# Performance work log

Hardware: AMD Instinct MI355X
Metric: run time of the kernel (lower is better)

The kernel has to match this reference:

```python
import jax, jax.numpy as jnp
import numpy as np

B, T, D, HS = 8, 2048, 768, 64
H = D // HS  # 12 heads
LN_EPS = 1e-5


def setup_inputs() -> dict:
    key = jax.random.key(0)
    ks = jax.random.split(key, 8)
    s = 0.02
    x = jax.random.normal(ks[0], (B, T, D), jnp.float32)
    Wx = jax.random.normal(ks[1], (D, D), jnp.float32) * s
    Ww = jax.random.normal(ks[2], (D, D), jnp.float32) * 0.01  # w_proj.weight ~ N(0,0.01)
    # w_proj bias schedule: logit(1 - linspace(0.9,0.999,H)) per head, expanded over head_size
    r_sched = jnp.linspace(0.9, 0.999, H)
    w_target = 1.0 - r_sched
    bw = jnp.log(w_target / (1.0 - w_target))          # logit
    bw = jnp.repeat(bw[:, None], HS, axis=1).reshape(-1)  # (D,)
    Wk = jax.random.normal(ks[3], (D, D), jnp.float32) * s
    Wv = jax.random.normal(ks[4], (D, D), jnp.float32) * s
    Wr = jax.random.normal(ks[5], (D, D), jnp.float32) * s
    Wo = jax.random.normal(ks[6], (D, D), jnp.float32) * s
    gamma = jnp.ones((D,), jnp.float32)
    beta = jnp.zeros((D,), jnp.float32)
    return {"x": x, "Wx": Wx, "Ww": Ww, "bw": bw, "Wk": Wk, "Wv": Wv,
            "Wr": Wr, "Wo": Wo, "gamma": gamma, "beta": beta}


def _layernorm(x, gamma, beta):
    mu = jnp.mean(x, axis=-1, keepdims=True)
    var = jnp.mean(jnp.square(x - mu), axis=-1, keepdims=True)
    return (x - mu) * jax.lax.rsqrt(var + LN_EPS) * gamma + beta


def _selective_scan(k, v, w):
    """k,v,w: (T,B,H,HS). State S: (B,H,HS,HS).
    S_t = (1 - w_t) * S_{t-1} (decay along key dim) + k_t (x) v_t;  y_t = k_t . S_t."""
    S0 = jnp.zeros((B, H, HS, HS), k.dtype)

    def step(S, inp):
        kt, vt, wt = inp  # each (B,H,HS)
        S = S * (1.0 - wt)[..., :, None] + kt[..., :, None] * vt[..., None, :]
        yt = jnp.einsum('bhi,bhij->bhj', kt, S)
        return S, yt

    _, ys = jax.lax.scan(step, S0, (k, v, w))
    return ys  # (T,B,H,HS)


def reference(x, Wx, Ww, bw, Wk, Wv, Wr, Wo, gamma, beta):
    xn = _layernorm(x, gamma, beta)                       # (B,T,D)
    xp = jnp.einsum('btd,ed->bte', xn, Wx)                # x_proj
    w = jax.nn.sigmoid(jnp.einsum('bte,fe->btf', xp, Ww) + bw)
    k = jnp.einsum('btd,ed->bte', xn, Wk)
    v = jnp.einsum('btd,ed->bte', xn, Wv)
    r = jax.nn.sigmoid(jnp.einsum('btd,ed->bte', xn, Wr))

    def to_scan(a):  # (B,T,D) -> (T,B,H,HS)
        return a.reshape(B, T, H, HS).transpose(1, 0, 2, 3)

    ys = _selective_scan(to_scan(k), to_scan(v), to_scan(w))  # (T,B,H,HS)
    y = ys.transpose(1, 0, 2, 3).reshape(B, T, D)
    y = y * r
    return jnp.einsum('btd,ed->bte', y, Wo)
```

## Files before the change

kernel.cpp:

```cpp
#include <hip/hip_runtime.h>

#define B_ 8
#define T_ 2048
#define D_ 768
#define H_ 12
#define HS_ 64
#define LN_EPS 1e-5f
#define NC 32
#define TC 64

typedef __attribute__((ext_vector_type(8))) short bf16x8;
typedef __attribute__((ext_vector_type(4))) float f32x4;

__device__ __forceinline__ ushort f2bf(float f) {
  unsigned u = __builtin_bit_cast(unsigned, f);
  unsigned r = (u + 0x7FFFu + ((u >> 16) & 1u)) >> 16;
  return (ushort)r;
}
__device__ __forceinline__ float bf2f(ushort u) {
  return __builtin_bit_cast(float, ((unsigned)u) << 16);
}

__device__ __forceinline__ int fragaddr(int t, int i) {
  return ((t >> 4) * 2 + (i >> 5)) * 512 + ((((i >> 3) & 3) * 16) + (t & 15)) * 8 + (i & 7);
}
__device__ __forceinline__ int fragswz(int i) {
  return (((i >> 3) & 3) << 3) ^ (((i >> 5) & 1) << 5);
}

__global__ __launch_bounds__(256) void zero_out_kernel(float* __restrict__ out, int n) {
  for (int i = blockIdx.x * 256 + threadIdx.x; i < n; i += gridDim.x * 256)
    out[i] = 0.f;
}

__global__ __launch_bounds__(256) void prep_kernel(
    const float* __restrict__ w0, const float* __restrict__ w1,
    const float* __restrict__ w2, const float* __restrict__ w3,
    const float* __restrict__ w4, const float* __restrict__ Wx,
    ushort* __restrict__ dst, ushort* __restrict__ WxT) {
  if (blockIdx.y < 5) {
    const float* srcs[5] = {w0, w1, w2, w3, w4};
    const int slots[5] = {0, 1, 2, 4, 5};
    const float* src = srcs[blockIdx.y];
    ushort* d = dst + (size_t)slots[blockIdx.y] * 589824;
    int idx = (blockIdx.x * 256 + threadIdx.x) * 4;
    float4 v = *reinterpret_cast<const float4*>(src + idx);
    ushort4 o;
    o.x = f2bf(v.x); o.y = f2bf(v.y); o.z = f2bf(v.z); o.w = f2bf(v.w);
    *reinterpret_cast<ushort4*>(d + idx) = o;
  } else {
    __shared__ ushort tile[32][33];
    const int bx = (blockIdx.x % 24) * 32;
    const int by = (blockIdx.x / 24) * 32;
    const int tx = threadIdx.x & 31, ty = threadIdx.x >> 5;
#pragma unroll
    for (int r = 0; r < 32; r += 8)
      tile[ty + r][tx] = f2bf(Wx[(size_t)(by + ty + r) * 768 + bx + tx]);
    __syncthreads();
#pragma unroll
    for (int r = 0; r < 32; r += 8)
      WxT[(size_t)(bx + ty + r) * 768 + by + tx] = tile[tx][ty + r];
  }
}

__global__ __launch_bounds__(256) void ln_kernel(
    const float* __restrict__ x, const float* __restrict__ gamma,
    const float* __restrict__ beta, ushort* __restrict__ xn) {
  const int wv = threadIdx.x >> 6;
  const int lane = threadIdx.x & 63;
  const int row = blockIdx.x * 4 + wv;
  const float* xr = x + (size_t)row * D_;
  float4 a[3];
#pragma unroll
  for (int s = 0; s < 3; ++s)
    a[s] = *reinterpret_cast<const float4*>(xr + s * 256 + lane * 4);
  float sum = 0.f;
#pragma unroll
  for (int s = 0; s < 3; ++s) sum += a[s].x + a[s].y + a[s].z + a[s].w;
#pragma unroll
  for (int off = 32; off; off >>= 1) sum += __shfl_xor(sum, off);
  float mu = sum * (1.f / 768.f);
  float vs = 0.f;
#pragma unroll
  for (int s = 0; s < 3; ++s) {
    float dx = a[s].x - mu, dy = a[s].y - mu, dz = a[s].z - mu, dw = a[s].w - mu;
    vs += dx * dx + dy * dy + dz * dz + dw * dw;
  }
#pragma unroll
  for (int off = 32; off; off >>= 1) vs += __shfl_xor(vs, off);
  float rs = rsqrtf(vs * (1.f / 768.f) + LN_EPS);
  ushort* orow = xn + (size_t)row * D_;
#pragma unroll
  for (int s = 0; s < 3; ++s) {
    int col = s * 256 + lane * 4;
    float4 g = *reinterpret_cast<const float4*>(gamma + col);
    float4 bb = *reinterpret_cast<const float4*>(beta + col);
    ushort4 o;
    o.x = f2bf((a[s].x - mu) * rs * g.x + bb.x);
    o.y = f2bf((a[s].y - mu) * rs * g.y + bb.y);
    o.z = f2bf((a[s].z - mu) * rs * g.z + bb.z);
    o.w = f2bf((a[s].w - mu) * rs * g.w + bb.w);
    *reinterpret_cast<ushort4*>(orow + col) = o;
  }
}

__global__ __launch_bounds__(512, 2) void gemm256(
    const ushort* __restrict__ A, const ushort* __restrict__ W,
    float* __restrict__ Cf,
    ushort* __restrict__ d0, ushort* __restrict__ d1,
    ushort* __restrict__ d2, ushort* __restrict__ d3, int mode) {
  __shared__ __align__(16) ushort lds[65536];
  const int tid = threadIdx.x;
  const int wid = tid >> 6;
  const int lane = tid & 63;
  const int wr = wid >> 2, wc = wid & 3;
  const int fr = lane & 15, fq = lane >> 4;
  const int m0 = blockIdx.x * 256, n0 = blockIdx.y * 256;
  const int strow = tid >> 3;
  const int stblk = tid & 7;

  const int RA0 = wr * 8192;
  const int RA1 = 32768 + wr * 8192;
  const int RB0 = 16384 + (wc >> 1) * 8192 + (wc & 1) * 4096;
  const int RB1 = 49152 + (wc >> 1) * 8192 + (wc & 1) * 4096;

  f32x4 acc[8][4];
#pragma unroll
  for (int m = 0; m < 8; ++m)
#pragma unroll
    for (int n = 0; n < 4; ++n) acc[m][n] = (f32x4){0.f, 0.f, 0.f, 0.f};

#define STAGE_HALF(gb, grow0, kk0, roff)                                          \
  {                                                                               \
    _Pragma("unroll") for (int j = 0; j < 2; ++j) {                               \
      const int lr_ = j * 64 + strow;                                             \
      const int bs_ = stblk ^ (lr_ & 7);                                          \
      const ushort* s_ = (gb) + (size_t)((grow0) + lr_) * 768 + (kk0) + bs_ * 8;  \
      __builtin_amdgcn_global_load_lds(                                           \
          (const __attribute__((address_space(1))) void*)s_,                      \
          (__attribute__((address_space(3))) void*)(lds + (roff) + j * 4096 + wid * 512), \
          16, 0, 0);                                                              \
    }                                                                             \
  }

#define LDF(dst, base, rf, kk)                                                    \
  dst = *reinterpret_cast<const bf16x8*>(                                         \
      lds + (base) + ((rf)*16 + fr) * 64 + ((((kk)*4 + fq) ^ (fr & 7)) * 8));

#define MFMA_Q(mb, nb, aa, bb)                                                    \
  _Pragma("unroll") for (int m_ = 0; m_ < 4; ++m_)                                \
  _Pragma("unroll") for (int n_ = 0; n_ < 2; ++n_)                                \
  _Pragma("unroll") for (int k_ = 0; k_ < 2; ++k_)                                \
    acc[(mb) + m_][(nb) + n_] = __builtin_amdgcn_mfma_f32_16x16x32_bf16(          \
        aa[m_][k_], bb[n_][k_], acc[(mb) + m_][(nb) + n_], 0, 0, 0);

#define LDF_AL(RA) \
  _Pragma("unroll") for (int m = 0; m < 4; ++m) { LDF(aL[m][0], RA, m, 0); LDF(aL[m][1], RA, m, 1); }
#define LDF_AH(RA) \
  _Pragma("unroll") for (int m = 0; m < 4; ++m) { LDF(aH[m][0], RA, m + 4, 0); LDF(aH[m][1], RA, m + 4, 1); }
#define LDF_BL(RB) \
  _Pragma("unroll") for (int n = 0; n < 2; ++n) { LDF(bL[n][0], RB, n, 0); LDF(bL[n][1], RB, n, 1); }
#define LDF_BH(RB) \
  _Pragma("unroll") for (int n = 0; n < 2; ++n) { LDF(bH[n][0], RB, n + 2, 0); LDF(bH[n][1], RB, n + 2, 1); }

  STAGE_HALF(A, m0, 0, 0);
  STAGE_HALF(A, m0 + 128, 0, 8192);
  STAGE_HALF(W, n0, 0, 16384);
  STAGE_HALF(W, n0 + 128, 0, 24576);
  STAGE_HALF(W, n0, 64, 49152);
  STAGE_HALF(W, n0 + 128, 64, 57344);
  asm volatile("s_waitcnt vmcnt(4)" ::: "memory");
  __builtin_amdgcn_s_barrier();

  bf16x8 aL[4][2], aH[4][2], bL[2][2], bH[2][2];

  for (int i = 0; i < 6; ++i) {
    const int kQ = (2 * i + 1) * 64;
    const int kP2 = (2 * i + 2 <= 11 ? 2 * i + 2 : 11) * 64;
    const int kQ2 = (2 * i + 3 <= 11 ? 2 * i + 3 : 11) * 64;

    STAGE_HALF(A, m0, kQ, 32768);
    STAGE_HALF(A, m0 + 128, kQ, 40960);
    LDF_AL(RA0);
    LDF_BL(RB0);
    LDF_BH(RB0);
    __builtin_amdgcn_s_barrier();
    __builtin_amdgcn_s_setprio(1);
    MFMA_Q(0, 0, aL, bL);
    MFMA_Q(0, 2, aL, bH);
    __builtin_amdgcn_s_setprio(0);
    __builtin_amdgcn_s_barrier();
    STAGE_HALF(W, n0, kP2, 16384);
    STAGE_HALF(W, n0 + 128, kP2, 24576);
    LDF_AH(RA0);
    __builtin_amdgcn_s_barrier();
    __builtin_amdgcn_s_setprio(1);
    MFMA_Q(4, 0, aH, bL);
    MFMA_Q(4, 2, aH, bH);
    __builtin_amdgcn_s_setprio(0);
    asm volatile("s_waitcnt vmcnt(4)" ::: "memory");
    __builtin_amdgcn_s_barrier();

    STAGE_HALF(A, m0, kP2, 0);
    STAGE_HALF(A, m0 + 128, kP2, 8192);
    LDF_AL(RA1);
    LDF_BL(RB1);
    LDF_BH(RB1);
    __builtin_amdgcn_s_barrier();
    __builtin_amdgcn_s_setprio(1);
    MFMA_Q(0, 0, aL, bL);
    MFMA_Q(0, 2, aL, bH);
    __builtin_amdgcn_s_setprio(0);
    __builtin_amdgcn_s_barrier();
    STAGE_HALF(W, n0, kQ2, 49152);
    STAGE_HALF(W, n0 + 128, kQ2, 57344);
    LDF_AH(RA1);
    __builtin_amdgcn_s_barrier();
    __builtin_amdgcn_s_setprio(1);
    MFMA_Q(4, 0, aH, bL);
    MFMA_Q(4, 2, aH, bH);
    __builtin_amdgcn_s_setprio(0);
    asm volatile("s_waitcnt vmcnt(4)" ::: "memory");
    __builtin_amdgcn_s_barrier();
  }

  const int r0 = fq * 4;
  if (mode == 5) {
    const int sel = n0 >= 2304 ? 3 : n0 >= 1536 ? 2 : n0 >= 768 ? 1 : 0;
    const int nb = n0 - sel * 768;
    if (sel == 1) {
#pragma unroll
      for (int mf = 0; mf < 8; ++mf)
#pragma unroll
        for (int nf = 0; nf < 4; ++nf) {
          int gr = m0 + wr * 128 + mf * 16 + r0;
          int gc = nb + wc * 64 + nf * 16 + fr;
          int b = gr >> 11, t = gr & 2047;
          int c = t >> 6, s0 = t & 63;
          int h = gc >> 6, j = gc & 63;
          size_t addr = ((size_t)((b * 12 + h) * 32 + c)) * 4096 +
                        (size_t)(((j >> 4) * 2 + (s0 >> 5)) * 512 +
                                 (((s0 >> 3) & 3) * 16 + (j & 15)) * 8 + (s0 & 7));
          ushort4 o;
          o.x = f2bf(acc[mf][nf][0]); o.y = f2bf(acc[mf][nf][1]);
          o.z = f2bf(acc[mf][nf][2]); o.w = f2bf(acc[mf][nf][3]);
          *reinterpret_cast<ushort4*>(d1 + addr) = o;
        }
    } else if (sel == 2) {
#pragma unroll
      for (int mf = 0; mf < 8; ++mf)
#pragma unroll
        for (int nf = 0; nf < 4; ++nf) {
          int gr = m0 + wr * 128 + mf * 16 + r0;
          int gc = nb + wc * 64 + nf * 16 + fr;
          int b = gr >> 11, t = gr & 2047;
          int c = t >> 6, tin = t & 63;
          int h = gc >> 6, j = gc & 63;
          size_t addr = ((size_t)((b * 12 + h) * 32 + c)) * 4096 +
                        (size_t)(((tin >> 4) * 64 + ((tin >> 2) & 3) * 16 + (j & 15)) * 16 +
                                 (j >> 4) * 4);
          ushort4 o;
          o.x = f2bf(1.f / (1.f + __expf(-acc[mf][nf][0])));
          o.y = f2bf(1.f / (1.f + __expf(-acc[mf][nf][1])));
          o.z = f2bf(1.f / (1.f + __expf(-acc[mf][nf][2])));
          o.w = f2bf(1.f / (1.f + __expf(-acc[mf][nf][3])));
          *reinterpret_cast<ushort4*>(d2 + addr) = o;
        }
    } else {
      ushort* dst = sel == 0 ? d0 : d3;
#pragma unroll
      for (int mf = 0; mf < 8; ++mf)
#pragma unroll
        for (int nf = 0; nf < 4; ++nf) {
          int gr = m0 + wr * 128 + mf * 16 + r0;
          int gc = nb + wc * 64 + nf * 16 + fr;
#pragma unroll
          for (int rr = 0; rr < 4; ++rr)
            dst[(size_t)(gr + rr) * 768 + gc] = f2bf(acc[mf][nf][rr]);
        }
    }
  } else {
#pragma unroll
    for (int mf = 0; mf < 8; ++mf)
#pragma unroll
      for (int nf = 0; nf < 4; ++nf) {
        int gr = m0 + wr * 128 + mf * 16 + r0;
        int gc = n0 + wc * 64 + nf * 16 + fr;
#pragma unroll
        for (int rr = 0; rr < 4; ++rr)
          Cf[(size_t)(gr + rr) * 768 + gc] = acc[mf][nf][rr];
      }
  }
#undef STAGE_HALF
#undef LDF
#undef MFMA_Q
#undef LDF_AL
#undef LDF_AH
#undef LDF_BL
#undef LDF_BH
}

__global__ __launch_bounds__(256) void scan_mc3(
    const ushort* __restrict__ kb, const ushort* __restrict__ zb,
    const ushort* __restrict__ vbF, const float* __restrict__ bwp,
    ushort* __restrict__ McT, float* __restrict__ aend) {
  __shared__ ushort kt[64 * 72];
  __shared__ ushort zt[64 * 72];
  __shared__ ushort kIAfA[4096];
  __shared__ float part[256];
  const int bh = blockIdx.x, c = blockIdx.y;
  const int b = bh / H_, h = bh % H_;
  const int tid = threadIdx.x;
  const int w = tid >> 6, lane = tid & 63;
  const int fr = lane & 15, fq = lane >> 4;
  const int row = tid >> 2, c16 = (tid & 3) * 16;
  const float bwh = bwp[h * 64];

  {
    const ushort* gk = kb + ((size_t)(b * T_ + c * TC + row)) * 768 + h * 64 + c16;
    const ushort* gz = zb + ((size_t)(b * T_ + c * TC + row)) * 768 + h * 64 + c16;
    uint4 k0 = *(const uint4*)gk, k1 = *(const uint4*)(gk + 8);
    uint4 z0 = *(const uint4*)gz, z1 = *(const uint4*)(gz + 8);
    *reinterpret_cast<uint4*>(&kt[row * 72 + c16]) = k0;
    *reinterpret_cast<uint4*>(&kt[row * 72 + c16 + 8]) = k1;
    *reinterpret_cast<uint4*>(&zt[row * 72 + c16]) = z0;
    *reinterpret_cast<uint4*>(&zt[row * 72 + c16 + 8]) = z1;
  }
  bf16x8 vfr[8];
  {
    const ushort* vch = vbF + ((size_t)bh * NC + c) * 4096;
#pragma unroll
    for (int f = 0; f < 8; ++f)
      vfr[f] = *reinterpret_cast<const bf16x8*>(vch + f * 512 + lane * 8);
  }
  __syncthreads();
  float dreg[16];
  float p = 1.f;
#pragma unroll
  for (int tt = 0; tt < 16; ++tt) {
    float z = bf2f(zt[(w * 16 + tt) * 72 + lane]);
    float d = 1.f / (1.f + __expf(z + bwh));
    dreg[tt] = d;
    p *= d;
  }
  part[w * 64 + lane] = p;
  __syncthreads();
  float a = 1.f;
  for (int w2 = 0; w2 < w; ++w2) a *= part[w2 * 64 + lane];
  if (w == 0)
    aend[((size_t)bh * NC + c) * 64 + lane] =
        part[lane] * part[64 + lane] * part[128 + lane] * part[192 + lane];
#pragma unroll
  for (int tt = 0; tt < 16; ++tt) {
    int t = w * 16 + tt;
    float k = bf2f(kt[t * 72 + lane]);
    a *= dreg[tt];
    kIAfA[fragaddr(lane, t)] = f2bf(k / a);
  }
  __syncthreads();

  bf16x8 af2[2];
#pragma unroll
  for (int kk = 0; kk < 2; ++kk)
    af2[kk] = *reinterpret_cast<const bf16x8*>(&kIAfA[(w * 2 + kk) * 512 + lane * 8]);
  f32x4 accM[4];
#pragma unroll
  for (int nf = 0; nf < 4; ++nf) accM[nf] = (f32x4){0.f, 0.f, 0.f, 0.f};
#pragma unroll
  for (int kk = 0; kk < 2; ++kk)
#pragma unroll
    for (int nf = 0; nf < 4; ++nf)
      accM[nf] = __builtin_amdgcn_mfma_f32_16x16x32_bf16(af2[kk], vfr[nf * 2 + kk], accM[nf], 0, 0, 0);
  ushort* mch = McT + ((size_t)bh * NC + c) * 4096;
#pragma unroll
  for (int nf = 0; nf < 4; ++nf) {
    ushort4 o;
    o.x = f2bf(accM[nf][0]); o.y = f2bf(accM[nf][1]);
    o.z = f2bf(accM[nf][2]); o.w = f2bf(accM[nf][3]);
    *reinterpret_cast<ushort4*>(&mch[(nf * 16 + fr) * 64 + w * 16 + fq * 4]) = o;
  }
}

__global__ __launch_bounds__(256) void scan_chain3(
    const ushort* __restrict__ McT, const float* __restrict__ aend,
    ushort* __restrict__ S0F) {
  const int bh = blockIdx.x;
  const int j = threadIdx.x >> 2;
  const int i0 = blockIdx.y * 32 + (threadIdx.x & 3) * 8;
  const int fbase = ((j >> 4) * 2 + (i0 >> 5)) * 512 + (((i0 >> 3) & 3) * 16 + (j & 15)) * 8;
  const ushort* mbase = McT + ((size_t)bh * NC) * 4096 + j * 64 + i0;
  const float* abase = aend + ((size_t)bh * NC) * 64 + i0;
  float S[8];
#pragma unroll
  for (int p = 0; p < 8; ++p) S[p] = 0.f;

  ushort4 m0 = *reinterpret_cast<const ushort4*>(mbase);
  ushort4 m1 = *reinterpret_cast<const ushort4*>(mbase + 4);
  float4 a0 = *(const float4*)(abase);
  float4 a1 = *(const float4*)(abase + 4);

  for (int c = 0; c < NC; ++c) {
    int cn = c + 1 < NC ? c + 1 : NC - 1;
    ushort4 n0 = *reinterpret_cast<const ushort4*>(mbase + (size_t)cn * 4096);
    ushort4 n1 = *reinterpret_cast<const ushort4*>(mbase + (size_t)cn * 4096 + 4);
    float4 b0 = *(const float4*)(abase + (size_t)cn * 64);
    float4 b1 = *(const float4*)(abase + (size_t)cn * 64 + 4);

    ushort* s0 = S0F + ((size_t)bh * NC + c) * 4096 + fbase;
    ushort4 o0, o1;
    o0.x = f2bf(S[0]); o0.y = f2bf(S[1]); o0.z = f2bf(S[2]); o0.w = f2bf(S[3]);
    o1.x = f2bf(S[4]); o1.y = f2bf(S[5]); o1.z = f2bf(S[6]); o1.w = f2bf(S[7]);
    *reinterpret_cast<ushort4*>(s0) = o0;
    *reinterpret_cast<ushort4*>(s0 + 4) = o1;

    S[0] = a0.x * (S[0] + bf2f(m0.x));
    S[1] = a0.y * (S[1] + bf2f(m0.y));
    S[2] = a0.z * (S[2] + bf2f(m0.z));
    S[3] = a0.w * (S[3] + bf2f(m0.w));
    S[4] = a1.x * (S[4] + bf2f(m1.x));
    S[5] = a1.y * (S[5] + bf2f(m1.y));
    S[6] = a1.z * (S[6] + bf2f(m1.z));
    S[7] = a1.w * (S[7] + bf2f(m1.w));

    m0 = n0; m1 = n1; a0 = b0; a1 = b1;
  }
}

__global__ __launch_bounds__(256, 2) void scan_y3(
    const ushort* __restrict__ kb, const ushort* __restrict__ zb,
    const ushort* __restrict__ vbF, const ushort* __restrict__ rbF,
    const ushort* __restrict__ S0F, const float* __restrict__ bwp,
    ushort* __restrict__ yrow) {
  __shared__ ushort kt[64 * 72];
  __shared__ ushort zt[64 * 72];
  __shared__ ushort kAf[4096];
  __shared__ ushort kIAfB[4096];
  __shared__ ushort Am[64 * 72];
  __shared__ float part[256];
  const int bh = blockIdx.x, c = blockIdx.y;
  const int b = bh / H_, h = bh % H_;
  const int tid = threadIdx.x;
  const int w = tid >> 6, lane = tid & 63;
  const int fr = lane & 15, fq = lane >> 4;
  const int row = tid >> 2, c16 = (tid & 3) * 16;
  const float bwh = bwp[h * 64];
  const int swz = fragswz(lane);

  {
    const ushort* gk = kb + ((size_t)(b * T_ + c * TC + row)) * 768 + h * 64 + c16;
    const ushort* gz = zb + ((size_t)(b * T_ + c * TC + row)) * 768 + h * 64 + c16;
    uint4 k0 = *(const uint4*)gk, k1 = *(const uint4*)(gk + 8);
    uint4 z0 = *(const uint4*)gz, z1 = *(const uint4*)(gz + 8);
    *reinterpret_cast<uint4*>(&kt[row * 72 + c16]) = k0;
    *reinterpret_cast<uint4*>(&kt[row * 72 + c16 + 8]) = k1;
    *reinterpret_cast<uint4*>(&zt[row * 72 + c16]) = z0;
    *reinterpret_cast<uint4*>(&zt[row * 72 + c16 + 8]) = z1;
  }
  bf16x8 vfr[8], s0fr[8];
  {
    const ushort* vch = vbF + ((size_t)bh * NC + c) * 4096;
    const ushort* s0ch = S0F + ((size_t)bh * NC + c) * 4096;
#pragma unroll
    for (int f = 0; f < 8; ++f) {
      vfr[f] = *reinterpret_cast<const bf16x8*>(vch + f * 512 + lane * 8);
      s0fr[f] = *reinterpret_cast<const bf16x8*>(s0ch + f * 512 + lane * 8);
    }
  }
  ushort4 rp0, rp1, rp2, rp3;
  {
    const ushort* rch = rbF + ((size_t)bh * NC + c) * 4096 + tid * 16;
    rp0 = *reinterpret_cast<const ushort4*>(rch);
    rp1 = *reinterpret_cast<const ushort4*>(rch + 4);
    rp2 = *reinterpret_cast<const ushort4*>(rch + 8);
    rp3 = *reinterpret_cast<const ushort4*>(rch + 12);
  }
  const ushort rl[16] = {rp0.x, rp0.y, rp0.z, rp0.w, rp1.x, rp1.y, rp1.z, rp1.w,
                         rp2.x, rp2.y, rp2.z, rp2.w, rp3.x, rp3.y, rp3.z, rp3.w};
  __syncthreads();
  float dreg[16];
  float p = 1.f;
#pragma unroll
  for (int tt = 0; tt < 16; ++tt) {
    float z = bf2f(zt[(w * 16 + tt) * 72 + lane]);
    float d = 1.f / (1.f + __expf(z + bwh));
    dreg[tt] = d;
    p *= d;
  }
  part[w * 64 + lane] = p;
  __syncthreads();
  float a = 1.f;
  for (int w2 = 0; w2 < w; ++w2) a *= part[w2 * 64 + lane];
#pragma unroll
  for (int tt = 0; tt < 16; ++tt) {
    int t = w * 16 + tt;
    float k = bf2f(kt[t * 72 + lane]);
    a *= dreg[tt];
    int ad = fragaddr(t, lane) ^ swz;
    kAf[ad] = f2bf(k * a);
    kIAfB[ad] = f2bf(k / a);
  }
  __syncthreads();

  bf16x8 af[2];
#pragma unroll
  for (int kk = 0; kk < 2; ++kk) {
    int ra = ((w * 2 + kk) * 512 + lane * 8) ^ (((lane >> 4) << 3) ^ (kk << 5));
    af[kk] = *reinterpret_cast<const bf16x8*>(&kAf[ra]);
  }
  {
    f32x4 accA[4];
#pragma unroll
    for (int nf = 0; nf < 4; ++nf) accA[nf] = (f32x4){0.f, 0.f, 0.f, 0.f};
#pragma unroll
    for (int kk = 0; kk < 2; ++kk)
#pragma unroll
      for (int nf = 0; nf < 4; ++nf) {
        int rb8 = ((nf * 2 + kk) * 512 + lane * 8) ^ (((lane >> 4) << 3) ^ (kk << 5));
        bf16x8 b8 = *reinterpret_cast<const bf16x8*>(&kIAfB[rb8]);
        accA[nf] = __builtin_amdgcn_mfma_f32_16x16x32_bf16(af[kk], b8, accA[nf], 0, 0, 0);
      }
#pragma unroll
    for (int nf = 0; nf < 4; ++nf)
#pragma unroll
      for (int q = 0; q < 4; ++q) {
        int t = w * 16 + fq * 4 + q;
        int s = nf * 16 + fr;
        Am[t * 72 + s] = f2bf((s <= t) ? accA[nf][q] : 0.f);
      }
  }
  __syncthreads();

  f32x4 accY[4];
#pragma unroll
  for (int nf = 0; nf < 4; ++nf) accY[nf] = (f32x4){0.f, 0.f, 0.f, 0.f};
#pragma unroll
  for (int kk = 0; kk < 2; ++kk)
#pragma unroll
    for (int nf = 0; nf < 4; ++nf)
      accY[nf] = __builtin_amdgcn_mfma_f32_16x16x32_bf16(af[kk], s0fr[nf * 2 + kk], accY[nf], 0, 0, 0);
#pragma unroll
  for (int kk = 0; kk < 2; ++kk) {
    bf16x8 am8 = *reinterpret_cast<const bf16x8*>(&Am[(w * 16 + fr) * 72 + kk * 32 + fq * 8]);
#pragma unroll
    for (int nf = 0; nf < 4; ++nf)
      accY[nf] = __builtin_amdgcn_mfma_f32_16x16x32_bf16(am8, vfr[nf * 2 + kk], accY[nf], 0, 0, 0);
  }
#pragma unroll
  for (int nf = 0; nf < 4; ++nf)
#pragma unroll
    for (int q = 0; q < 4; ++q) {
      int t = w * 16 + fq * 4 + q;
      int j = nf * 16 + fr;
      size_t go = ((size_t)(b * T_ + c * TC + t)) * 768 + h * 64 + j;
      yrow[go] = f2bf(accY[nf][q] * bf2f(rl[nf * 4 + q]));
    }
}

extern "C" void kernel_launch(void* const* d_in, const int* in_sizes, int n_in,
                              void* d_out, int out_size, void* d_ws, size_t ws_size,
                              hipStream_t stream) {
  const float* x     = (const float*)d_in[0];
  const float* Wx    = (const float*)d_in[1];
  const float* Ww    = (const float*)d_in[2];
  const float* bw    = (const float*)d_in[3];
  const float* Wk    = (const float*)d_in[4];
  const float* Wv    = (const float*)d_in[5];
  const float* Wr    = (const float*)d_in[6];
  const float* Wo    = (const float*)d_in[7];
  const float* gamma = (const float*)d_in[8];
  const float* beta  = (const float*)d_in[9];
  float* out = (float*)d_out;

  const size_t NEED = 208404480ull;
  if (ws_size < NEED) {
    zero_out_kernel<<<2048, 256, 0, stream>>>(out, out_size);
    return;
  }

  char* ws = (char*)d_ws;
  ushort* xn  = (ushort*)ws;
  ushort* wb  = (ushort*)(ws + 25165824);
  ushort* WxT = (ushort*)(ws + 32243712);
  ushort* kb  = (ushort*)(ws + 57409536);
  ushort* vbF = (ushort*)(ws + 82575360);
  ushort* rbF = (ushort*)(ws + 107741184);
  ushort* yr  = (ushort*)(ws + 132907008);
  ushort* zb  = (ushort*)(ws + 158072832);
  ushort* McT = (ushort*)ws;
  ushort* S0F = (ushort*)(ws + 32243712);
  float*  aendb = (float*)(ws + 132907008);

  ushort* WcatB = wb;
  ushort* Mb  = wb + 3 * 589824;
  ushort* WoB = wb + 4 * 589824;
  ushort* WwB = wb + 5 * 589824;

  prep_kernel<<<dim3(576, 6), 256, 0, stream>>>(Wk, Wv, Wr, Wo, Ww, Wx, wb, WxT);
  gemm256<<<dim3(3, 3), 512, 0, stream>>>(WwB, WxT, nullptr, Mb, nullptr, nullptr,
                                          nullptr, 5);
  ln_kernel<<<4096, 256, 0, stream>>>(x, gamma, beta, xn);

  gemm256<<<dim3(64, 12), 512, 0, stream>>>(xn, WcatB, nullptr, kb, vbF, rbF, zb, 5);

  scan_mc3<<<dim3(96, NC), 256, 0, stream>>>(kb, zb, vbF, bw, McT, aendb);
  scan_chain3<<<dim3(96, 2), 256, 0, stream>>>(McT, aendb, S0F);
  scan_y3<<<dim3(96, NC), 256, 0, stream>>>(kb, zb, vbF, rbF, S0F, bw, yr);

  gemm256<<<dim3(64, 3), 512, 0, stream>>>(yr, WoB, out, nullptr, nullptr, nullptr,
                                           nullptr, 0);
}
```

Before: 227.7 us.

## Replace 256x256 GEMM with 128x256 tile, K=32 double-buffered pipeline

Rewrites the shared GEMM kernel to use a 128x256 output tile per block with a smaller K step of 32, a simple two-stage LDS double buffer, and XOR-swizzled 4-segment rows. This cuts LDS from 128KB to 48KB and accumulator registers by half, targeting more blocks per CU and more blocks overall to fill the GPU better (e.g. 1536 vs 768 blocks for the main projection). In exchange it gives up the software-pipelined quarter-step schedule and reuses each operand fragment over fewer MFMAs, which raises LDS traffic per flop and adds more barriers.

```diff
diff --git a/kernel.cpp b/kernel.cpp
--- a/kernel.cpp
+++ b/kernel.cpp
@@ -104,125 +104,81 @@
   }
 }
 
-__global__ __launch_bounds__(512, 2) void gemm256(
+__global__ __launch_bounds__(512, 4) void gemm_p(
     const ushort* __restrict__ A, const ushort* __restrict__ W,
     float* __restrict__ Cf,
     ushort* __restrict__ d0, ushort* __restrict__ d1,
     ushort* __restrict__ d2, ushort* __restrict__ d3, int mode) {
-  __shared__ __align__(16) ushort lds[65536];
+  __shared__ __align__(16) ushort lds[24576];
   const int tid = threadIdx.x;
   const int wid = tid >> 6;
   const int lane = tid & 63;
   const int wr = wid >> 2, wc = wid & 3;
   const int fr = lane & 15, fq = lane >> 4;
-  const int m0 = blockIdx.x * 256, n0 = blockIdx.y * 256;
-  const int strow = tid >> 3;
-  const int stblk = tid & 7;
-
-  const int RA0 = wr * 8192;
-  const int RA1 = 32768 + wr * 8192;
-  const int RB0 = 16384 + (wc >> 1) * 8192 + (wc & 1) * 4096;
-  const int RB1 = 49152 + (wc >> 1) * 8192 + (wc & 1) * 4096;
-
-  f32x4 acc[8][4];
-#pragma unroll
-  for (int m = 0; m < 8; ++m)
+  const int m0 = blockIdx.x * 128, n0 = blockIdx.y * 256;
+  const int strow = tid >> 2;
+  const int stseg = (tid & 3) ^ (strow & 3);
+  const int rseg = fq ^ (fr & 3);
+
+  f32x4 acc[4][4];
+#pragma unroll
+  for (int m = 0; m < 4; ++m)
 #pragma unroll
     for (int n = 0; n < 4; ++n) acc[m][n] = (f32x4){0.f, 0.f, 0.f, 0.f};
 
-#define STAGE_HALF(gb, grow0, kk0, roff)                                          \
+#define STAGE_T(kk0, b)                                                           \
   {                                                                               \
+    const ushort* sa_ = A + (size_t)(m0 + strow) * 768 + (kk0) + stseg * 8;       \
+    __builtin_amdgcn_global_load_lds(                                             \
+        (const __attribute__((address_space(1))) void*)sa_,                       \
+        (__attribute__((address_space(3))) void*)(lds + (b) * 4096 + tid * 8),    \
+        16, 0, 0);                                                                \
     _Pragma("unroll") for (int j = 0; j < 2; ++j) {                               \
-      const int lr_ = j * 64 + strow;                                             \
-      const int bs_ = stblk ^ (lr_ & 7);                                          \
-      const ushort* s_ = (gb) + (size_t)((grow0) + lr_) * 768 + (kk0) + bs_ * 8;  \
+      const ushort* sb_ =                                                         \
+          W + (size_t)(n0 + j * 128 + strow) * 768 + (kk0) + stseg * 8;           \
       __builtin_amdgcn_global_load_lds(                                           \
-          (const __attribute__((address_space(1))) void*)s_,                      \
-          (__attribute__((address_space(3))) void*)(lds + (roff) + j * 4096 + wid * 512), \
+          (const __attribute__((address_space(1))) void*)sb_,                     \
+          (__attribute__((address_space(3))) void*)(lds + 8192 + (b) * 8192 +     \
+                                                    j * 4096 + tid * 8),          \
           16, 0, 0);                                                              \
     }                                                                             \
   }
 
-#define LDF(dst, base, rf, kk)                                                    \
-  dst = *reinterpret_cast<const bf16x8*>(                                         \
-      lds + (base) + ((rf)*16 + fr) * 64 + ((((kk)*4 + fq) ^ (fr & 7)) * 8));
-
-#define MFMA_Q(mb, nb, aa, bb)                                                    \
-  _Pragma("unroll") for (int m_ = 0; m_ < 4; ++m_)                                \
-  _Pragma("unroll") for (int n_ = 0; n_ < 2; ++n_)                                \
-  _Pragma("unroll") for (int k_ = 0; k_ < 2; ++k_)                                \
-    acc[(mb) + m_][(nb) + n_] = __builtin_amdgcn_mfma_f32_16x16x32_bf16(          \
-        aa[m_][k_], bb[n_][k_], acc[(mb) + m_][(nb) + n_], 0, 0, 0);
-
-#define LDF_AL(RA) \
-  _Pragma("unroll") for (int m = 0; m < 4; ++m) { LDF(aL[m][0], RA, m, 0); LDF(aL[m][1], RA, m, 1); }
-#define LDF_AH(RA) \
-  _Pragma("unroll") for (int m = 0; m < 4; ++m) { LDF(aH[m][0], RA, m + 4, 0); LDF(aH[m][1], RA, m + 4, 1); }
-#define LDF_BL(RB) \
-  _Pragma("unroll") for (int n = 0; n < 2; ++n) { LDF(bL[n][0], RB, n, 0); LDF(bL[n][1], RB, n, 1); }
-#define LDF_BH(RB) \
-  _Pragma("unroll") for (int n = 0; n < 2; ++n) { LDF(bH[n][0], RB, n + 2, 0); LDF(bH[n][1], RB, n + 2, 1); }
-
-  STAGE_HALF(A, m0, 0, 0);
-  STAGE_HALF(A, m0 + 128, 0, 8192);
-  STAGE_HALF(W, n0, 0, 16384);
-  STAGE_HALF(W, n0 + 128, 0, 24576);
-  STAGE_HALF(W, n0, 64, 49152);
-  STAGE_HALF(W, n0 + 128, 64, 57344);
-  asm volatile("s_waitcnt vmcnt(4)" ::: "memory");
+  STAGE_T(0, 0);
+  STAGE_T(32, 1);
+  asm volatile("s_waitcnt vmcnt(3)" ::: "memory");
   __builtin_amdgcn_s_barrier();
 
-  bf16x8 aL[4][2], aH[4][2], bL[2][2], bH[2][2];
-
-  for (int i = 0; i < 6; ++i) {
-    const int kQ = (2 * i + 1) * 64;
-    const int kP2 = (2 * i + 2 <= 11 ? 2 * i + 2 : 11) * 64;
-    const int kQ2 = (2 * i + 3 <= 11 ? 2 * i + 3 : 11) * 64;
-
-    STAGE_HALF(A, m0, kQ, 32768);
-    STAGE_HALF(A, m0 + 128, kQ, 40960);
-    LDF_AL(RA0);
-    LDF_BL(RB0);
-    LDF_BH(RB0);
-    __builtin_amdgcn_s_barrier();
+#pragma unroll 2
+  for (int t = 0; t < 24; ++t) {
+    const int cur = t & 1;
+    bf16x8 aF[4], bF[4];
+#pragma unroll
+    for (int mi = 0; mi < 4; ++mi)
+      aF[mi] = *reinterpret_cast<const bf16x8*>(
+          lds + cur * 4096 + (wr * 64 + mi * 16 + fr) * 32 + rseg * 8);
+#pragma unroll
+    for (int nf = 0; nf < 4; ++nf)
+      bF[nf] = *reinterpret_cast<const bf16x8*>(
+          lds + 8192 + cur * 8192 + (wc * 64 + nf * 16 + fr) * 32 + rseg * 8);
     __builtin_amdgcn_s_setprio(1);
-    MFMA_Q(0, 0, aL, bL);
-    MFMA_Q(0, 2, aL, bH);
+#pragma unroll
+    for (int mi = 0; mi < 4; ++mi)
+#pragma unroll
+      for (int nf = 0; nf < 4; ++nf)
+        acc[mi][nf] = __builtin_amdgcn_mfma_f32_16x16x32_bf16(
+            aF[mi], bF[nf], acc[mi][nf], 0, 0, 0);
     __builtin_amdgcn_s_setprio(0);
     __builtin_amdgcn_s_barrier();
-    STAGE_HALF(W, n0, kP2, 16384);
-    STAGE_HALF(W, n0 + 128, kP2, 24576);
-    LDF_AH(RA0);
+    if (t + 2 < 24) {
+      STAGE_T((t + 2) * 32, cur);
+      asm volatile("s_waitcnt vmcnt(3)" ::: "memory");
+    } else {
+      asm volatile("s_waitcnt vmcnt(0)" ::: "memory");
+    }
     __builtin_amdgcn_s_barrier();
-    __builtin_amdgcn_s_setprio(1);
-    MFMA_Q(4, 0, aH, bL);
-    MFMA_Q(4, 2, aH, bH);
-    __builtin_amdgcn_s_setprio(0);
-    asm volatile("s_waitcnt vmcnt(4)" ::: "memory");
-    __builtin_amdgcn_s_barrier();
-
-    STAGE_HALF(A, m0, kP2, 0);
-    STAGE_HALF(A, m0 + 128, kP2, 8192);
-    LDF_AL(RA1);
-    LDF_BL(RB1);
-    LDF_BH(RB1);
-    __builtin_amdgcn_s_barrier();
-    __builtin_amdgcn_s_setprio(1);
-    MFMA_Q(0, 0, aL, bL);
-    MFMA_Q(0, 2, aL, bH);
-    __builtin_amdgcn_s_setprio(0);
-    __builtin_amdgcn_s_barrier();
-    STAGE_HALF(W, n0, kQ2, 49152);
-    STAGE_HALF(W, n0 + 128, kQ2, 57344);
-    LDF_AH(RA1);
-    __builtin_amdgcn_s_barrier();
-    __builtin_amdgcn_s_setprio(1);
-    MFMA_Q(4, 0, aH, bL);
-    MFMA_Q(4, 2, aH, bH);
-    __builtin_amdgcn_s_setprio(0);
-    asm volatile("s_waitcnt vmcnt(4)" ::: "memory");
-    __builtin_amdgcn_s_barrier();
-  }
+  }
+#undef STAGE_T
 
   const int r0 = fq * 4;
   if (mode == 5) {
@@ -230,10 +186,10 @@
     const int nb = n0 - sel * 768;
     if (sel == 1) {
 #pragma unroll
-      for (int mf = 0; mf < 8; ++mf)
+      for (int mf = 0; mf < 4; ++mf)
 #pragma unroll
         for (int nf = 0; nf < 4; ++nf) {
-          int gr = m0 + wr * 128 + mf * 16 + r0;
+          int gr = m0 + wr * 64 + mf * 16 + r0;
           int gc = nb + wc * 64 + nf * 16 + fr;
           int b = gr >> 11, t = gr & 2047;
           int c = t >> 6, s0 = t & 63;
@@ -248,10 +204,10 @@
         }
     } else if (sel == 2) {
 #pragma unroll
-      for (int mf = 0; mf < 8; ++mf)
+      for (int mf = 0; mf < 4; ++mf)
 #pragma unroll
         for (int nf = 0; nf < 4; ++nf) {
-          int gr = m0 + wr * 128 + mf * 16 + r0;
+          int gr = m0 + wr * 64 + mf * 16 + r0;
           int gc = nb + wc * 64 + nf * 16 + fr;
           int b = gr >> 11, t = gr & 2047;
           int c = t >> 6, tin = t & 63;
@@ -269,10 +225,10 @@
     } else {
       ushort* dst = sel == 0 ? d0 : d3;
 #pragma unroll
-      for (int mf = 0; mf < 8; ++mf)
+      for (int mf = 0; mf < 4; ++mf)
 #pragma unroll
         for (int nf = 0; nf < 4; ++nf) {
-          int gr = m0 + wr * 128 + mf * 16 + r0;
+          int gr = m0 + wr * 64 + mf * 16 + r0;
           int gc = nb + wc * 64 + nf * 16 + fr;
 #pragma unroll
           for (int rr = 0; rr < 4; ++rr)
@@ -281,23 +237,16 @@
     }
   } else {
 #pragma unroll
-    for (int mf = 0; mf < 8; ++mf)
+    for (int mf = 0; mf < 4; ++mf)
 #pragma unroll
       for (int nf = 0; nf < 4; ++nf) {
-        int gr = m0 + wr * 128 + mf * 16 + r0;
+        int gr = m0 + wr * 64 + mf * 16 + r0;
         int gc = n0 + wc * 64 + nf * 16 + fr;
 #pragma unroll
         for (int rr = 0; rr < 4; ++rr)
           Cf[(size_t)(gr + rr) * 768 + gc] = acc[mf][nf][rr];
       }
   }
-#undef STAGE_HALF
-#undef LDF
-#undef MFMA_Q
-#undef LDF_AL
-#undef LDF_AH
-#undef LDF_BL
-#undef LDF_BH
 }
 
 __global__ __launch_bounds__(256) void scan_mc3(
@@ -596,16 +545,16 @@
   ushort* WwB = wb + 5 * 589824;
 
   prep_kernel<<<dim3(576, 6), 256, 0, stream>>>(Wk, Wv, Wr, Wo, Ww, Wx, wb, WxT);
-  gemm256<<<dim3(3, 3), 512, 0, stream>>>(WwB, WxT, nullptr, Mb, nullptr, nullptr,
-                                          nullptr, 5);
+  gemm_p<<<dim3(6, 3), 512, 0, stream>>>(WwB, WxT, nullptr, Mb, nullptr, nullptr,
+                                         nullptr, 5);
   ln_kernel<<<4096, 256, 0, stream>>>(x, gamma, beta, xn);
 
-  gemm256<<<dim3(64, 12), 512, 0, stream>>>(xn, WcatB, nullptr, kb, vbF, rbF, zb, 5);
+  gemm_p<<<dim3(128, 12), 512, 0, stream>>>(xn, WcatB, nullptr, kb, vbF, rbF, zb, 5);
 
   scan_mc3<<<dim3(96, NC), 256, 0, stream>>>(kb, zb, vbF, bw, McT, aendb);
   scan_chain3<<<dim3(96, 2), 256, 0, stream>>>(McT, aendb, S0F);
   scan_y3<<<dim3(96, NC), 256, 0, stream>>>(kb, zb, vbF, rbF, S0F, bw, yr);
 
-  gemm256<<<dim3(64, 3), 512, 0, stream>>>(yr, WoB, out, nullptr, nullptr, nullptr,
+  gemm_p<<<dim3(128, 3), 512, 0, stream>>>(yr, WoB, out, nullptr, nullptr, nullptr,
                                            nullptr, 0);
 }
```

New measurement: 230.0 us. About the same (+1.0%).
